# Kernel optimization log

Measured on AMD Instinct MI355X. Metric: run time of the kernel, lower is better.

## Reference

```python
import jax, jax.numpy as jnp
import numpy as np

N, E, IN, HID, OUT = 50000, 800000, 128, 64, 32
ALPHA, BETA, DIVIDER = 0.5, 0.5, 5.0


def _gcn_conv(x, edge_index, W, b, alpha=ALPHA, beta=BETA):
    """DirectedGCNConv.forward: add self loops, linear, degree-normalized gather-mul-scatter."""
    n = x.shape[0]
    loops = jnp.arange(n, dtype=edge_index.dtype)
    row = jnp.concatenate([edge_index[0], loops])  # sources
    col = jnp.concatenate([edge_index[1], loops])  # targets
    x = x @ W.T + b                                # [n, out]
    ones = jnp.ones(row.shape[0], dtype=x.dtype)
    in_deg = jax.ops.segment_sum(ones, col, num_segments=n)
    out_deg = jax.ops.segment_sum(ones, row, num_segments=n)
    norm = in_deg[col] ** (-alpha) * out_deg[row] ** (-beta)  # [E+n]
    msgs = norm[:, None] * x[row]                  # gather + scale
    return jax.ops.segment_sum(msgs, col, num_segments=n)  # scatter-add aggr


def _source_enc(x, ei, W1, b1, W2, b2):
    x = jax.nn.relu(_gcn_conv(x, ei, W1, b1))
    return _gcn_conv(x, jnp.flip(ei, axis=0), W2, b2)


def _target_enc(x, ei, W1, b1, W2, b2):
    x = jax.nn.relu(_gcn_conv(x, jnp.flip(ei, axis=0), W1, b1))
    return _gcn_conv(x, ei, W2, b2)


def setup_inputs() -> dict:
    key = jax.random.key(0)
    ks = jax.random.split(key, 24)

    def lin(kw, kb, o, i, scale):
        return (jax.random.normal(kw, (o, i), jnp.float32) * scale,
                jax.random.normal(kb, (o,), jnp.float32) * 0.01)

    s1 = (2.0 / (IN + HID)) ** 0.5
    s2 = (2.0 / (HID + OUT)) ** 0.5
    inp = {
        "s": jax.random.normal(ks[0], (N, IN), jnp.float32),
        "t": jax.random.normal(ks[1], (N, IN), jnp.float32),
        "edge_index": jax.random.randint(ks[2], (2, E), 0, N, jnp.int32),
        "noise_s": jax.random.normal(ks[3], (N, OUT), jnp.float32),
        "noise_t": jax.random.normal(ks[4], (N, OUT), jnp.float32),
    }
    names = ["sm", "sl", "tm", "tl"]  # source/target mu/logstd encoders
    k = 5
    for nm in names:
        W1, b1 = lin(ks[k], ks[k + 1], HID, IN, s1); k += 2
        W2, b2 = lin(ks[k], ks[k + 1], OUT, HID, s2); k += 2
        inp[nm + "1_W"], inp[nm + "1_b"] = W1, b1
        inp[nm + "2_W"], inp[nm + "2_b"] = W2, b2
    return inp


def reference(s, t, edge_index, noise_s, noise_t,
              sm1_W, sm1_b, sm2_W, sm2_b,
              sl1_W, sl1_b, sl2_W, sl2_b,
              tm1_W, tm1_b, tm2_W, tm2_b,
              tl1_W, tl1_b, tl2_W, tl2_b):
    s_mu = _source_enc(s, edge_index, sm1_W, sm1_b, sm2_W, sm2_b)
    s_logstd = _source_enc(s, edge_index, sl1_W, sl1_b, sl2_W, sl2_b)
    t_mu = _target_enc(t, edge_index, tm1_W, tm1_b, tm2_W, tm2_b)
    t_logstd = _target_enc(t, edge_index, tl1_W, tl1_b, tl2_W, tl2_b)
    # reparametrize_edges (training mode), noise materialized as input
    s_out = s_mu + noise_s * jnp.exp(s_logstd) / DIVIDER
    t_out = t_mu + noise_t * jnp.exp(t_logstd) / DIVIDER
    return (s_out, t_out)
```

## Files before the change

### kernel.cpp

```cpp
#include <hip/hip_runtime.h>
#include <hip/hip_fp16.h>
#include <math.h>

#define N_NODES 50000
#define E_EDGES 800000
#define NCHUNKS ((N_NODES + 1023) / 1024)
#define LIN_BLOCKS 1564
#define CNT_BLOCKS 3125

typedef _Float16 half8 __attribute__((ext_vector_type(8)));
typedef float f32x4 __attribute__((ext_vector_type(4)));

__device__ inline float fac_from(unsigned int u) {
    unsigned short us = (unsigned short)(u >> 16);
    __half h;
    __builtin_memcpy(&h, &us, 2);
    return __half2float(h);
}

__global__ __launch_bounds__(256) void zero2_kernel(int* a, int* b, int n) {
    int t = blockIdx.x * 256 + threadIdx.x;
    if (t < n) { a[t] = 0; b[t] = 0; }
}

__global__ __launch_bounds__(256) void count_lin1_kernel(const int* __restrict__ ei0,
                                                         const int* __restrict__ ei1,
                                                         int* cnt_fwd, int* cnt_bwd,
                                                         int* rank_fwd, int* rank_bwd,
                                                         const float* __restrict__ Xs,
                                                         const float* __restrict__ Xt,
                                                         const float* __restrict__ sWa,
                                                         const float* __restrict__ sba,
                                                         const float* __restrict__ sWb,
                                                         const float* __restrict__ sbb,
                                                         const float* __restrict__ tWa,
                                                         const float* __restrict__ tba,
                                                         const float* __restrict__ tWb,
                                                         const float* __restrict__ tbb,
                                                         __half* __restrict__ As,
                                                         __half* __restrict__ At, int n) {
    int bx = blockIdx.x;
    int tid = threadIdx.x;
    if (bx % 3 != 1) {
        int cidx = (bx / 3) * 2 + (bx % 3 == 2 ? 1 : 0);
        if (cidx >= CNT_BLOCKS) return;
        int t = cidx * 256 + tid;
        if (t < E_EDGES) {
            rank_fwd[t] = atomicAdd(&cnt_fwd[ei1[t]], 1);
            rank_bwd[t] = atomicAdd(&cnt_bwd[ei0[t]], 1);
        }
        return;
    }
    int lidx = bx / 3;
    int y = lidx & 1;
    int xb = lidx >> 1;
    const float* X = y ? Xt : Xs;
    const float* Wset[2] = { y ? tWa : sWa, y ? tWb : sWb };
    const float* bset[2] = { y ? tba : sba, y ? tbb : sbb };
    __half* A = y ? At : As;

    int w = tid >> 6, lane = tid & 63;
    int quad = lane >> 4, col = lane & 15;
    int node0 = xb * 64 + w * 16;

    half8 afrag[4];
    {
        int row = node0 + col;
        if (row >= n) row = n - 1;
        const float* xr = X + (size_t)row * 128 + quad * 8;
#pragma unroll
        for (int kc = 0; kc < 4; ++kc) {
            float4 f0 = *(const float4*)(xr + kc * 32);
            float4 f1 = *(const float4*)(xr + kc * 32 + 4);
            half8 h;
            h[0] = (_Float16)f0.x; h[1] = (_Float16)f0.y;
            h[2] = (_Float16)f0.z; h[3] = (_Float16)f0.w;
            h[4] = (_Float16)f1.x; h[5] = (_Float16)f1.y;
            h[6] = (_Float16)f1.z; h[7] = (_Float16)f1.w;
            afrag[kc] = h;
        }
    }

#pragma unroll
    for (int set = 0; set < 2; ++set) {
        const float* Ws = Wset[set];
#pragma unroll
        for (int nt = 0; nt < 4; ++nt) {
            float bb = bset[set][nt * 16 + col];
            f32x4 acc = { bb, bb, bb, bb };
            const float* wr = Ws + (size_t)(nt * 16 + col) * 128 + quad * 8;
#pragma unroll
            for (int kc = 0; kc < 4; ++kc) {
                float4 f0 = *(const float4*)(wr + kc * 32);
                float4 f1 = *(const float4*)(wr + kc * 32 + 4);
                half8 bfr;
                bfr[0] = (_Float16)f0.x; bfr[1] = (_Float16)f0.y;
                bfr[2] = (_Float16)f0.z; bfr[3] = (_Float16)f0.w;
                bfr[4] = (_Float16)f1.x; bfr[5] = (_Float16)f1.y;
                bfr[6] = (_Float16)f1.z; bfr[7] = (_Float16)f1.w;
                acc = __builtin_amdgcn_mfma_f32_16x16x32_f16(afrag[kc], bfr, acc, 0, 0, 0);
            }
#pragma unroll
            for (int r = 0; r < 4; ++r) {
                int node = node0 + quad * 4 + r;
                if (node < n)
                    A[(size_t)node * 128 + set * 64 + nt * 16 + col] = __float2half(acc[r]);
            }
        }
    }
}

__global__ __launch_bounds__(1024) void scan_chunk2_kernel(const int* __restrict__ cnt_f,
                                                           const int* __restrict__ cnt_b,
                                                           int* __restrict__ offs_f,
                                                           int* __restrict__ offs_b,
                                                           int* __restrict__ part_f,
                                                           int* __restrict__ part_b, int n) {
    const int* cnt = blockIdx.y ? cnt_b : cnt_f;
    int* offs = blockIdx.y ? offs_b : offs_f;
    int* partials = blockIdx.y ? part_b : part_f;
    __shared__ int sh[1024];
    int tid = threadIdx.x;
    int i = blockIdx.x * 1024 + tid;
    int v = (i < n) ? cnt[i] : 0;
    sh[tid] = v;
    __syncthreads();
    for (int off = 1; off < 1024; off <<= 1) {
        int add = (tid >= off) ? sh[tid - off] : 0;
        __syncthreads();
        sh[tid] += add;
        __syncthreads();
    }
    if (i < n) offs[i] = sh[tid] - v;
    if (tid == 1023) partials[blockIdx.x] = sh[tid];
}

__global__ __launch_bounds__(64) void scan_partials2_kernel(int* part_f, int* part_b, int nchunks) {
    int* p = blockIdx.x ? part_b : part_f;
    __shared__ int sh[64];
    int tid = threadIdx.x;
    int v = (tid < nchunks) ? p[tid] : 0;
    sh[tid] = v;
    __syncthreads();
    for (int off = 1; off < 64; off <<= 1) {
        int add = (tid >= off) ? sh[tid - off] : 0;
        __syncthreads();
        sh[tid] += add;
        __syncthreads();
    }
    if (tid < nchunks) p[tid] = sh[tid] - v;
    if (tid == 63) p[nchunks] = sh[63];
}

__global__ __launch_bounds__(256) void addback_deg_kernel(int* __restrict__ offs_f,
                                                          int* __restrict__ offs_b,
                                                          const int* __restrict__ part_f,
                                                          const int* __restrict__ part_b,
                                                          const int* __restrict__ cnt_f,
                                                          const int* __restrict__ cnt_b,
                                                          float* dsi, float* dti,
                                                          int n, int nchunks) {
    int i = blockIdx.x * 256 + threadIdx.x;
    if (blockIdx.y == 0) {
        if (i < n) {
            offs_f[i] += part_f[i >> 10];
            dti[i] = rsqrtf((float)(cnt_f[i] + 1));
        } else if (i == n) offs_f[n] = part_f[nchunks];
    } else {
        if (i < n) {
            offs_b[i] += part_b[i >> 10];
            dsi[i] = rsqrtf((float)(cnt_b[i] + 1));
        } else if (i == n) offs_b[n] = part_b[nchunks];
    }
}

__global__ __launch_bounds__(256) void fill2_kernel(const int* __restrict__ ei0,
                                                    const int* __restrict__ ei1,
                                                    const int* __restrict__ rank_f,
                                                    const int* __restrict__ rank_b,
                                                    const int* __restrict__ offs_f,
                                                    const int* __restrict__ offs_b,
                                                    const float* __restrict__ dsi,
                                                    const float* __restrict__ dti,
                                                    unsigned int* __restrict__ pay_f,
                                                    unsigned int* __restrict__ pay_b, int e) {
    int t = blockIdx.x * 256 + threadIdx.x;
    if (t >= e) return;
    if (blockIdx.y == 0) {
        int id = ei0[t];
        __half h = __float2half(dsi[id]);
        unsigned short hb; __builtin_memcpy(&hb, &h, 2);
        pay_f[offs_f[ei1[t]] + rank_f[t]] = (unsigned int)id | ((unsigned int)hb << 16);
    } else {
        int id = ei1[t];
        __half h = __float2half(dti[id]);
        unsigned short hb; __builtin_memcpy(&hb, &h, 2);
        pay_b[offs_b[ei0[t]] + rank_b[t]] = (unsigned int)id | ((unsigned int)hb << 16);
    }
}

__device__ inline void acc_fma(float* acc, uint4 u, float f) {
    const __half2* h = (const __half2*)&u;
    float2 f0 = __half22float2(h[0]);
    float2 f1 = __half22float2(h[1]);
    float2 f2 = __half22float2(h[2]);
    float2 f3 = __half22float2(h[3]);
    acc[0] += f * f0.x; acc[1] += f * f0.y; acc[2] += f * f1.x; acc[3] += f * f1.y;
    acc[4] += f * f2.x; acc[5] += f * f2.y; acc[6] += f * f3.x; acc[7] += f * f3.y;
}

__global__ __launch_bounds__(256) void pull_lin2_kernel(const __half* __restrict__ As,
                                                        const __half* __restrict__ At,
                                                        __half* __restrict__ Cs,
                                                        __half* __restrict__ Ct,
                                                        const int* __restrict__ offs_f,
                                                        const int* __restrict__ offs_b,
                                                        const unsigned int* __restrict__ pay_f,
                                                        const unsigned int* __restrict__ pay_b,
                                                        const float* __restrict__ dsi,
                                                        const float* __restrict__ dti,
                                                        const float* __restrict__ sW2a,
                                                        const float* __restrict__ sb2a,
                                                        const float* __restrict__ sW2b,
                                                        const float* __restrict__ sb2b,
                                                        const float* __restrict__ tW2a,
                                                        const float* __restrict__ tb2a,
                                                        const float* __restrict__ tW2b,
                                                        const float* __restrict__ tb2b, int n) {
    int y = blockIdx.y;
    const __half* xw = y ? At : As;
    __half* C = y ? Ct : Cs;
    const int* offs = y ? offs_b : offs_f;
    const unsigned int* pay = y ? pay_b : pay_f;
    const float* fac_self  = y ? dsi : dti;
    const float* fac_other = y ? dti : dsi;
    const float* W2a = y ? tW2a : sW2a;  const float* b2a = y ? tb2a : sb2a;
    const float* W2b = y ? tW2b : sW2b;  const float* b2b = y ? tb2b : sb2b;

    __shared__ float Wt[64 * 66];
    __shared__ float bsh[64];
    __shared__ float xs[16 * 132];

    int tid = threadIdx.x;
    for (int idx = tid; idx < 2048; idx += 256) {
        int o = idx >> 6, k = idx & 63;
        Wt[k * 66 + o]      = W2a[idx];
        Wt[k * 66 + 33 + o] = W2b[idx];
    }
    if (tid < 32) { bsh[tid] = b2a[tid]; bsh[32 + tid] = b2b[tid]; }

    int ln = tid >> 4;
    int f4 = tid & 15;
    int v = blockIdx.x * 16 + ln;
    int i = offs[v], end = offs[v + 1];
    const uint4* xw16 = (const uint4*)xw;

    float acc[8] = {0, 0, 0, 0, 0, 0, 0, 0};
    acc_fma(acc, xw16[v * 16 + f4], fac_other[v]);
    while (i < end && (i & 3)) {
        unsigned int pk = pay[i];
        acc_fma(acc, xw16[(pk & 0xffff) * 16 + f4], fac_from(pk));
        ++i;
    }
    for (; i + 3 < end; i += 4) {
        uint4 pk = *(const uint4*)(pay + i);
        int s0 = pk.x & 0xffff, s1 = pk.y & 0xffff;
        int s2 = pk.z & 0xffff, s3 = pk.w & 0xffff;
        uint4 ua = xw16[s0 * 16 + f4];
        uint4 ub = xw16[s1 * 16 + f4];
        uint4 uc = xw16[s2 * 16 + f4];
        uint4 ud = xw16[s3 * 16 + f4];
        acc_fma(acc, ua, fac_from(pk.x));
        acc_fma(acc, ub, fac_from(pk.y));
        acc_fma(acc, uc, fac_from(pk.z));
        acc_fma(acc, ud, fac_from(pk.w));
    }
    for (; i < end; ++i) {
        unsigned int pk = pay[i];
        acc_fma(acc, xw16[(pk & 0xffff) * 16 + f4], fac_from(pk));
    }

    float fs = fac_self[v];
    float4 a0, a1;
    a0.x = fmaxf(acc[0] * fs, 0.0f); a0.y = fmaxf(acc[1] * fs, 0.0f);
    a0.z = fmaxf(acc[2] * fs, 0.0f); a0.w = fmaxf(acc[3] * fs, 0.0f);
    a1.x = fmaxf(acc[4] * fs, 0.0f); a1.y = fmaxf(acc[5] * fs, 0.0f);
    a1.z = fmaxf(acc[6] * fs, 0.0f); a1.w = fmaxf(acc[7] * fs, 0.0f);
    *(float4*)&xs[ln * 132 + f4 * 8]     = a0;
    *(float4*)&xs[ln * 132 + f4 * 8 + 4] = a1;
    __syncthreads();

    int nn = tid >> 5, o = tid & 31;
    const float* x0 = &xs[nn * 132];
    const float* x1 = &xs[(nn + 8) * 132];
    float am0 = bsh[o], al0 = bsh[32 + o];
    float am1 = am0,    al1 = al0;
#pragma unroll 4
    for (int k = 0; k < 64; ++k) {
        float wm = Wt[k * 66 + o], wl = Wt[k * 66 + 33 + o];
        am0 += x0[k] * wm;  al0 += x0[64 + k] * wl;
        am1 += x1[k] * wm;  al1 += x1[64 + k] * wl;
    }
    int v0 = blockIdx.x * 16 + nn;
    int v1 = v0 + 8;
    C[v0 * 64 + o]      = __float2half(am0);
    C[v0 * 64 + 32 + o] = __float2half(al0);
    C[v1 * 64 + o]      = __float2half(am1);
    C[v1 * 64 + 32 + o] = __float2half(al1);
}

__global__ __launch_bounds__(256) void final_pull2_kernel(const __half* __restrict__ Cs,
                                                          const __half* __restrict__ Ct,
                                                          float* __restrict__ out_s,
                                                          float* __restrict__ out_t,
                                                          const int* __restrict__ offs_f,
                                                          const int* __restrict__ offs_b,
                                                          const unsigned int* __restrict__ pay_f,
                                                          const unsigned int* __restrict__ pay_b,
                                                          const float* __restrict__ dsi,
                                                          const float* __restrict__ dti,
                                                          const float* __restrict__ noise_s,
                                                          const float* __restrict__ noise_t,
                                                          int n) {
    int y = blockIdx.y;
    const __half* xw = y ? Ct : Cs;
    float* out = y ? out_t : out_s;
    const int* offs = y ? offs_f : offs_b;
    const unsigned int* pay = y ? pay_f : pay_b;
    const float* fac_self  = y ? dti : dsi;
    const float* fac_other = y ? dsi : dti;
    const float* noise = y ? noise_t : noise_s;

    const uint4* xw16 = (const uint4*)xw;
    int ln = threadIdx.x >> 3;
    int f4 = threadIdx.x & 7;
    int v = blockIdx.x * 32 + ln;
    if (v >= n) return;
    int i = offs[v], end = offs[v + 1];

    float acc[8] = {0, 0, 0, 0, 0, 0, 0, 0};
    acc_fma(acc, xw16[v * 8 + f4], fac_other[v]);
    while (i < end && (i & 3)) {
        unsigned int pk = pay[i];
        acc_fma(acc, xw16[(pk & 0xffff) * 8 + f4], fac_from(pk));
        ++i;
    }
    for (; i + 3 < end; i += 4) {
        uint4 pk = *(const uint4*)(pay + i);
        int s0 = pk.x & 0xffff, s1 = pk.y & 0xffff;
        int s2 = pk.z & 0xffff, s3 = pk.w & 0xffff;
        uint4 ua = xw16[s0 * 8 + f4];
        uint4 ub = xw16[s1 * 8 + f4];
        uint4 uc = xw16[s2 * 8 + f4];
        uint4 ud = xw16[s3 * 8 + f4];
        acc_fma(acc, ua, fac_from(pk.x));
        acc_fma(acc, ub, fac_from(pk.y));
        acc_fma(acc, uc, fac_from(pk.z));
        acc_fma(acc, ud, fac_from(pk.w));
    }
    for (; i < end; ++i) {
        unsigned int pk = pay[i];
        acc_fma(acc, xw16[(pk & 0xffff) * 8 + f4], fac_from(pk));
    }

    float fs = fac_self[v];
#pragma unroll
    for (int j = 0; j < 8; ++j) acc[j] *= fs;

    int lane = threadIdx.x & 63;
    float lg[8];
#pragma unroll
    for (int j = 0; j < 8; ++j) lg[j] = __shfl(acc[j], lane + 4);
    if (f4 < 4) {
        const float4* nz4 = (const float4*)noise;
        float4 n0 = nz4[v * 8 + f4 * 2];
        float4 n1 = nz4[v * 8 + f4 * 2 + 1];
        float4 r0, r1;
        r0.x = acc[0] + n0.x * expf(lg[0]) * 0.2f;
        r0.y = acc[1] + n0.y * expf(lg[1]) * 0.2f;
        r0.z = acc[2] + n0.z * expf(lg[2]) * 0.2f;
        r0.w = acc[3] + n0.w * expf(lg[3]) * 0.2f;
        r1.x = acc[4] + n1.x * expf(lg[4]) * 0.2f;
        r1.y = acc[5] + n1.y * expf(lg[5]) * 0.2f;
        r1.z = acc[6] + n1.z * expf(lg[6]) * 0.2f;
        r1.w = acc[7] + n1.w * expf(lg[7]) * 0.2f;
        float4* o4 = (float4*)out;
        o4[v * 8 + f4 * 2]     = r0;
        o4[v * 8 + f4 * 2 + 1] = r1;
    }
}

extern "C" void kernel_launch(void* const* d_in, const int* in_sizes, int n_in,
                              void* d_out, int out_size, void* d_ws, size_t ws_size,
                              hipStream_t stream) {
    const float* s       = (const float*)d_in[0];
    const float* t       = (const float*)d_in[1];
    const int*   ei      = (const int*)d_in[2];
    const float* noise_s = (const float*)d_in[3];
    const float* noise_t = (const float*)d_in[4];
    const float* sm1_W = (const float*)d_in[5];  const float* sm1_b = (const float*)d_in[6];
    const float* sm2_W = (const float*)d_in[7];  const float* sm2_b = (const float*)d_in[8];
    const float* sl1_W = (const float*)d_in[9];  const float* sl1_b = (const float*)d_in[10];
    const float* sl2_W = (const float*)d_in[11]; const float* sl2_b = (const float*)d_in[12];
    const float* tm1_W = (const float*)d_in[13]; const float* tm1_b = (const float*)d_in[14];
    const float* tm2_W = (const float*)d_in[15]; const float* tm2_b = (const float*)d_in[16];
    const float* tl1_W = (const float*)d_in[17]; const float* tl1_b = (const float*)d_in[18];
    const float* tl2_W = (const float*)d_in[19]; const float* tl2_b = (const float*)d_in[20];

    const int* ei0 = ei;
    const int* ei1 = ei + E_EDGES;

    __half* A_s = (__half*)d_ws;
    __half* A_t = A_s + (size_t)N_NODES * 128;
    __half* C_s = A_t + (size_t)N_NODES * 128;
    __half* C_t = C_s + (size_t)N_NODES * 64;
    unsigned int* pay_fwd = (unsigned int*)(C_t + (size_t)N_NODES * 64);
    unsigned int* pay_bwd = pay_fwd + E_EDGES;
    float* dsi = (float*)(pay_bwd + E_EDGES);
    float* dti = dsi + N_NODES;
    int* offs_fwd = (int*)(dti + N_NODES);
    int* offs_bwd = offs_fwd + N_NODES + 1;
    int* cnt_fwd  = offs_bwd + N_NODES + 1;
    int* cnt_bwd  = cnt_fwd + N_NODES;
    int* rank_fwd = cnt_bwd + N_NODES;
    int* rank_bwd = rank_fwd + E_EDGES;
    int* part_fwd = rank_bwd + E_EDGES;
    int* part_bwd = part_fwd + NCHUNKS + 1;

    float* s_out = (float*)d_out;
    float* t_out = (float*)d_out + N_NODES * 32;

    dim3 blk(256);
    int ngrid = (N_NODES + 255) / 256;
    int egrid = (E_EDGES + 255) / 256;
    dim3 agrid((N_NODES + 1 + 255) / 256, 2);
    dim3 pgrid(N_NODES / 16, 2);
    dim3 fgrid((N_NODES + 31) / 32, 2);

    zero2_kernel<<<ngrid, blk, 0, stream>>>(cnt_fwd, cnt_bwd, N_NODES);
    count_lin1_kernel<<<3 * LIN_BLOCKS, blk, 0, stream>>>(
        ei0, ei1, cnt_fwd, cnt_bwd, rank_fwd, rank_bwd,
        s, t, sm1_W, sm1_b, sl1_W, sl1_b, tm1_W, tm1_b, tl1_W, tl1_b,
        A_s, A_t, N_NODES);
    scan_chunk2_kernel<<<dim3(NCHUNKS, 2), 1024, 0, stream>>>(
        cnt_fwd, cnt_bwd, offs_fwd, offs_bwd, part_fwd, part_bwd, N_NODES);
    scan_partials2_kernel<<<2, 64, 0, stream>>>(part_fwd, part_bwd, NCHUNKS);
    addback_deg_kernel<<<agrid, blk, 0, stream>>>(offs_fwd, offs_bwd, part_fwd, part_bwd,
                                                  cnt_fwd, cnt_bwd, dsi, dti,
                                                  N_NODES, NCHUNKS);
    fill2_kernel<<<dim3(egrid, 2), blk, 0, stream>>>(ei0, ei1, rank_fwd, rank_bwd,
                                                     offs_fwd, offs_bwd, dsi, dti,
                                                     pay_fwd, pay_bwd, E_EDGES);

    pull_lin2_kernel<<<pgrid, blk, 0, stream>>>(A_s, A_t, C_s, C_t,
                                                offs_fwd, offs_bwd, pay_fwd, pay_bwd,
                                                dsi, dti,
                                                sm2_W, sm2_b, sl2_W, sl2_b,
                                                tm2_W, tm2_b, tl2_W, tl2_b, N_NODES);
    final_pull2_kernel<<<fgrid, blk, 0, stream>>>(C_s, C_t, s_out, t_out,
                                                  offs_fwd, offs_bwd, pay_fwd, pay_bwd,
                                                  dsi, dti, noise_s, noise_t, N_NODES);
}
```

Before: 361.8 us.

## Replace global-atomic CSR build with per-chunk LDS histograms and prefix ranks

```diff
diff --git a/kernel.cpp b/kernel.cpp
--- a/kernel.cpp
+++ b/kernel.cpp
@@ -3,10 +3,12 @@
 #include <math.h>
 
 #define N_NODES 50000
+#define NPACK 25000
 #define E_EDGES 800000
 #define NCHUNKS ((N_NODES + 1023) / 1024)
 #define LIN_BLOCKS 1564
-#define CNT_BLOCKS 3125
+#define QCH 64
+#define CHUNK (E_EDGES / QCH)
 
 typedef _Float16 half8 __attribute__((ext_vector_type(8)));
 typedef float f32x4 __attribute__((ext_vector_type(4)));
@@ -18,40 +20,25 @@
     return __half2float(h);
 }
 
-__global__ __launch_bounds__(256) void zero2_kernel(int* a, int* b, int n) {
-    int t = blockIdx.x * 256 + threadIdx.x;
-    if (t < n) { a[t] = 0; b[t] = 0; }
-}
-
-__global__ __launch_bounds__(256) void count_lin1_kernel(const int* __restrict__ ei0,
-                                                         const int* __restrict__ ei1,
-                                                         int* cnt_fwd, int* cnt_bwd,
-                                                         int* rank_fwd, int* rank_bwd,
-                                                         const float* __restrict__ Xs,
-                                                         const float* __restrict__ Xt,
-                                                         const float* __restrict__ sWa,
-                                                         const float* __restrict__ sba,
-                                                         const float* __restrict__ sWb,
-                                                         const float* __restrict__ sbb,
-                                                         const float* __restrict__ tWa,
-                                                         const float* __restrict__ tba,
-                                                         const float* __restrict__ tWb,
-                                                         const float* __restrict__ tbb,
-                                                         __half* __restrict__ As,
-                                                         __half* __restrict__ At, int n) {
-    int bx = blockIdx.x;
-    int tid = threadIdx.x;
-    if (bx % 3 != 1) {
-        int cidx = (bx / 3) * 2 + (bx % 3 == 2 ? 1 : 0);
-        if (cidx >= CNT_BLOCKS) return;
-        int t = cidx * 256 + tid;
-        if (t < E_EDGES) {
-            rank_fwd[t] = atomicAdd(&cnt_fwd[ei1[t]], 1);
-            rank_bwd[t] = atomicAdd(&cnt_bwd[ei0[t]], 1);
-        }
-        return;
-    }
-    int lidx = bx / 3;
+__device__ inline int unpack_cnt(const unsigned int* cntp, int i) {
+    unsigned int w = cntp[i >> 1];
+    return (i & 1) ? (int)(w >> 16) : (int)(w & 0xffff);
+}
+
+__global__ __launch_bounds__(256) void lin1_kernel(const float* __restrict__ Xs,
+                                                   const float* __restrict__ Xt,
+                                                   const float* __restrict__ sWa,
+                                                   const float* __restrict__ sba,
+                                                   const float* __restrict__ sWb,
+                                                   const float* __restrict__ sbb,
+                                                   const float* __restrict__ tWa,
+                                                   const float* __restrict__ tba,
+                                                   const float* __restrict__ tWb,
+                                                   const float* __restrict__ tbb,
+                                                   __half* __restrict__ As,
+                                                   __half* __restrict__ At, int n) {
+    int lidx = blockIdx.x;
+    int tid = threadIdx.x;
     int y = lidx & 1;
     int xb = lidx >> 1;
     const float* X = y ? Xt : Xs;
@@ -110,19 +97,54 @@
     }
 }
 
-__global__ __launch_bounds__(1024) void scan_chunk2_kernel(const int* __restrict__ cnt_f,
-                                                           const int* __restrict__ cnt_b,
+__global__ __launch_bounds__(256) void hist_kernel(const int* __restrict__ ei0,
+                                                   const int* __restrict__ ei1,
+                                                   unsigned int* __restrict__ ghist) {
+    __shared__ unsigned int h[NPACK];
+    int q = blockIdx.x, dir = blockIdx.y;
+    int tid = threadIdx.x;
+    for (int i = tid; i < NPACK; i += 256) h[i] = 0;
+    __syncthreads();
+    const int* key = dir ? ei0 : ei1;
+    int base = q * CHUNK;
+    for (int i = base + tid; i < base + CHUNK; i += 256) {
+        int v = key[i];
+        atomicAdd(&h[v >> 1], 1u << ((v & 1) * 16));
+    }
+    __syncthreads();
+    unsigned int* g = ghist + (size_t)(dir * QCH + q) * NPACK;
+    for (int i = tid; i < NPACK; i += 256) g[i] = h[i];
+}
+
+__global__ __launch_bounds__(256) void nodescan_kernel(unsigned int* __restrict__ ghist,
+                                                       unsigned int* __restrict__ cntp) {
+    int vp = blockIdx.x * 256 + threadIdx.x;
+    int dir = blockIdx.y;
+    if (vp >= NPACK) return;
+    unsigned int lo = 0, hi = 0;
+    unsigned int* g = ghist + (size_t)dir * QCH * NPACK + vp;
+#pragma unroll 4
+    for (int q = 0; q < QCH; ++q) {
+        unsigned int w = g[(size_t)q * NPACK];
+        g[(size_t)q * NPACK] = lo | (hi << 16);
+        lo += w & 0xffff;
+        hi += w >> 16;
+    }
+    cntp[dir * NPACK + vp] = lo | (hi << 16);
+}
+
+__global__ __launch_bounds__(1024) void scan_chunk2_kernel(const unsigned int* __restrict__ cntp,
                                                            int* __restrict__ offs_f,
                                                            int* __restrict__ offs_b,
                                                            int* __restrict__ part_f,
                                                            int* __restrict__ part_b, int n) {
-    const int* cnt = blockIdx.y ? cnt_b : cnt_f;
+    const unsigned int* cnt = cntp + (blockIdx.y ? NPACK : 0);
     int* offs = blockIdx.y ? offs_b : offs_f;
     int* partials = blockIdx.y ? part_b : part_f;
     __shared__ int sh[1024];
     int tid = threadIdx.x;
     int i = blockIdx.x * 1024 + tid;
-    int v = (i < n) ? cnt[i] : 0;
+    int v = (i < n) ? unpack_cnt(cnt, i) : 0;
     sh[tid] = v;
     __syncthreads();
     for (int off = 1; off < 1024; off <<= 1) {
@@ -156,46 +178,54 @@
                                                           int* __restrict__ offs_b,
                                                           const int* __restrict__ part_f,
                                                           const int* __restrict__ part_b,
-                                                          const int* __restrict__ cnt_f,
-                                                          const int* __restrict__ cnt_b,
+                                                          const unsigned int* __restrict__ cntp,
                                                           float* dsi, float* dti,
                                                           int n, int nchunks) {
     int i = blockIdx.x * 256 + threadIdx.x;
     if (blockIdx.y == 0) {
         if (i < n) {
             offs_f[i] += part_f[i >> 10];
-            dti[i] = rsqrtf((float)(cnt_f[i] + 1));
+            dti[i] = rsqrtf((float)(unpack_cnt(cntp, i) + 1));
         } else if (i == n) offs_f[n] = part_f[nchunks];
     } else {
         if (i < n) {
             offs_b[i] += part_b[i >> 10];
-            dsi[i] = rsqrtf((float)(cnt_b[i] + 1));
+            dsi[i] = rsqrtf((float)(unpack_cnt(cntp + NPACK, i) + 1));
         } else if (i == n) offs_b[n] = part_b[nchunks];
     }
 }
 
-__global__ __launch_bounds__(256) void fill2_kernel(const int* __restrict__ ei0,
-                                                    const int* __restrict__ ei1,
-                                                    const int* __restrict__ rank_f,
-                                                    const int* __restrict__ rank_b,
-                                                    const int* __restrict__ offs_f,
-                                                    const int* __restrict__ offs_b,
-                                                    const float* __restrict__ dsi,
-                                                    const float* __restrict__ dti,
-                                                    unsigned int* __restrict__ pay_f,
-                                                    unsigned int* __restrict__ pay_b, int e) {
-    int t = blockIdx.x * 256 + threadIdx.x;
-    if (t >= e) return;
-    if (blockIdx.y == 0) {
-        int id = ei0[t];
-        __half h = __float2half(dsi[id]);
-        unsigned short hb; __builtin_memcpy(&hb, &h, 2);
-        pay_f[offs_f[ei1[t]] + rank_f[t]] = (unsigned int)id | ((unsigned int)hb << 16);
-    } else {
-        int id = ei1[t];
-        __half h = __float2half(dti[id]);
-        unsigned short hb; __builtin_memcpy(&hb, &h, 2);
-        pay_b[offs_b[ei0[t]] + rank_b[t]] = (unsigned int)id | ((unsigned int)hb << 16);
+__global__ __launch_bounds__(256) void fill_lds_kernel(const int* __restrict__ ei0,
+                                                       const int* __restrict__ ei1,
+                                                       const unsigned int* __restrict__ ghist,
+                                                       const int* __restrict__ offs_f,
+                                                       const int* __restrict__ offs_b,
+                                                       const float* __restrict__ dsi,
+                                                       const float* __restrict__ dti,
+                                                       unsigned int* __restrict__ pay_f,
+                                                       unsigned int* __restrict__ pay_b) {
+    __shared__ unsigned int h[NPACK];
+    int q = blockIdx.x, dir = blockIdx.y;
+    int tid = threadIdx.x;
+    for (int i = tid; i < NPACK; i += 256) h[i] = 0;
+    __syncthreads();
+    const int* key = dir ? ei0 : ei1;
+    const int* pid = dir ? ei1 : ei0;
+    const float* fac = dir ? dti : dsi;
+    const int* offs = dir ? offs_b : offs_f;
+    unsigned int* pay = dir ? pay_b : pay_f;
+    const unsigned int* pref = ghist + (size_t)(dir * QCH + q) * NPACK;
+    int base = q * CHUNK;
+    for (int i = base + tid; i < base + CHUNK; i += 256) {
+        int v = key[i];
+        int sh = (v & 1) * 16;
+        unsigned int old = atomicAdd(&h[v >> 1], 1u << sh);
+        int rank = (int)((old >> sh) & 0xffff);
+        int cb = (int)((pref[v >> 1] >> sh) & 0xffff);
+        int id = pid[i];
+        __half hf = __float2half(fac[id]);
+        unsigned short hb; __builtin_memcpy(&hb, &hf, 2);
+        pay[offs[v] + cb + rank] = (unsigned int)id | ((unsigned int)hb << 16);
     }
 }
 
@@ -420,37 +450,35 @@
     float* dti = dsi + N_NODES;
     int* offs_fwd = (int*)(dti + N_NODES);
     int* offs_bwd = offs_fwd + N_NODES + 1;
-    int* cnt_fwd  = offs_bwd + N_NODES + 1;
-    int* cnt_bwd  = cnt_fwd + N_NODES;
-    int* rank_fwd = cnt_bwd + N_NODES;
-    int* rank_bwd = rank_fwd + E_EDGES;
-    int* part_fwd = rank_bwd + E_EDGES;
+    unsigned int* cntp = (unsigned int*)(offs_bwd + N_NODES + 1);
+    int* part_fwd = (int*)(cntp + 2 * NPACK);
     int* part_bwd = part_fwd + NCHUNKS + 1;
+
+    unsigned int* ghist = (unsigned int*)C_s;
 
     float* s_out = (float*)d_out;
     float* t_out = (float*)d_out + N_NODES * 32;
 
     dim3 blk(256);
-    int ngrid = (N_NODES + 255) / 256;
-    int egrid = (E_EDGES + 255) / 256;
     dim3 agrid((N_NODES + 1 + 255) / 256, 2);
     dim3 pgrid(N_NODES / 16, 2);
     dim3 fgrid((N_NODES + 31) / 32, 2);
-
-    zero2_kernel<<<ngrid, blk, 0, stream>>>(cnt_fwd, cnt_bwd, N_NODES);
-    count_lin1_kernel<<<3 * LIN_BLOCKS, blk, 0, stream>>>(
-        ei0, ei1, cnt_fwd, cnt_bwd, rank_fwd, rank_bwd,
+    dim3 hgrid(QCH, 2);
+    dim3 nsgrid((NPACK + 255) / 256, 2);
+
+    lin1_kernel<<<LIN_BLOCKS, blk, 0, stream>>>(
         s, t, sm1_W, sm1_b, sl1_W, sl1_b, tm1_W, tm1_b, tl1_W, tl1_b,
         A_s, A_t, N_NODES);
+
+    hist_kernel<<<hgrid, blk, 0, stream>>>(ei0, ei1, ghist);
+    nodescan_kernel<<<nsgrid, blk, 0, stream>>>(ghist, cntp);
     scan_chunk2_kernel<<<dim3(NCHUNKS, 2), 1024, 0, stream>>>(
-        cnt_fwd, cnt_bwd, offs_fwd, offs_bwd, part_fwd, part_bwd, N_NODES);
+        cntp, offs_fwd, offs_bwd, part_fwd, part_bwd, N_NODES);
     scan_partials2_kernel<<<2, 64, 0, stream>>>(part_fwd, part_bwd, NCHUNKS);
     addback_deg_kernel<<<agrid, blk, 0, stream>>>(offs_fwd, offs_bwd, part_fwd, part_bwd,
-                                                  cnt_fwd, cnt_bwd, dsi, dti,
-                                                  N_NODES, NCHUNKS);
-    fill2_kernel<<<dim3(egrid, 2), blk, 0, stream>>>(ei0, ei1, rank_fwd, rank_bwd,
-                                                     offs_fwd, offs_bwd, dsi, dti,
-                                                     pay_fwd, pay_bwd, E_EDGES);
+                                                  cntp, dsi, dti, N_NODES, NCHUNKS);
+    fill_lds_kernel<<<hgrid, blk, 0, stream>>>(ei0, ei1, ghist, offs_fwd, offs_bwd,
+                                               dsi, dti, pay_fwd, pay_bwd);
 
     pull_lin2_kernel<<<pgrid, blk, 0, stream>>>(A_s, A_t, C_s, C_t,
                                                 offs_fwd, offs_bwd, pay_fwd, pay_bwd,
```

Measured after the change: 383.4 us. +6.0%, slower.
